# Performance work log

Hardware: AMD Instinct MI355X
Metric: run time of the kernel (lower is better)

## Reference

```python
import jax, jax.numpy as jnp
import numpy as np

TOP_K = 10
RANKING_WEIGHT = 0.3
UP_WEIGHT = 1.0
DOWN_WEIGHT = 0.5
NEG = 1e9  # finite stand-in for -inf so softmax/grads stay NaN-free


def setup_inputs() -> dict:
    key = jax.random.key(0)
    k1, k2, k3, k4 = jax.random.split(key, 4)
    B, N = 1024, 5000
    up_logits = jax.random.normal(k1, (B, N), jnp.float32)
    down_logits = jax.random.normal(k2, (B, N), jnp.float32)
    y_true = jax.random.normal(k3, (B, N), jnp.float32) * 0.05  # daily returns
    masks = jax.random.randint(k4, (B, N), 0, 2).astype(jnp.int32)
    return {"up_logits": up_logits, "down_logits": down_logits,
            "y_true": y_true, "masks": masks}


def _bce_with_logits(x, z):
    # softplus(x) - x*z  ==  -[z*log(sig(x)) + (1-z)*log(1-sig(x))]
    return jax.nn.softplus(x) - x * z


def reference(up_logits, down_logits, y_true, masks):
    maskb = masks > 0                                   # [B, N]
    maskf = maskb.astype(up_logits.dtype)
    num_valid = maskf.sum(-1)                           # [B]
    nv_safe = jnp.maximum(num_valid, 1.0)
    k = jnp.minimum(TOP_K, num_valid.astype(jnp.int32))  # [B] min(top_k, num)

    # Descending rank of y_true among valid entries (invalid pushed to bottom).
    y_desc = jnp.where(maskb, y_true, -NEG)
    rank_desc = jnp.argsort(jnp.argsort(-y_desc, axis=-1), axis=-1)  # [B, N]
    up_labels = (rank_desc < k[:, None]).astype(up_logits.dtype)

    # Ascending rank (biggest losers) for down path.
    y_asc = jnp.where(maskb, y_true, NEG)
    rank_asc = jnp.argsort(jnp.argsort(y_asc, axis=-1), axis=-1)
    down_labels = (rank_asc < k[:, None]).astype(down_logits.dtype)

    # Mean BCE over valid entries per row.
    up_loss = jnp.sum(_bce_with_logits(up_logits, up_labels) * maskf, -1) / nv_safe
    down_loss = jnp.sum(_bce_with_logits(down_logits, down_labels) * maskf, -1) / nv_safe

    # Listwise KL: softmax over valid entries; kl_div(log p, q, 'batchmean')
    # with 1D input of size num divides the sum by num.
    logp = jax.nn.log_softmax(jnp.where(maskb, up_logits, -NEG), axis=-1)
    logq = jax.nn.log_softmax(jnp.where(maskb, y_true, -NEG), axis=-1)
    q = jnp.exp(logq)
    kl = jnp.sum(jnp.where(maskb, q * (logq - logp), 0.0), -1) / nv_safe

    batch_loss = UP_WEIGHT * up_loss + DOWN_WEIGHT * down_loss + RANKING_WEIGHT * kl
    batch_loss = jnp.where(num_valid > 0, batch_loss, 0.0)  # skip empty rows
    return jnp.sum(batch_loss) / up_logits.shape[0]
```

## Files before the change

### kernel.cpp

```cpp
#include <hip/hip_runtime.h>
#include <math.h>

#define NCOLS 5000
#define NF4   1250
#define BLOCK 640
#define NWAVES (BLOCK / 64)
#define NITER 2
#define TOPKK 10
#define CAP 384

__device__ __forceinline__ unsigned mono_f32(float f) {
  unsigned u = __float_as_uint(f);
  return (u & 0x80000000u) ? ~u : (u | 0x80000000u);
}

__device__ __forceinline__ float wave_sum_f(float v) {
#pragma unroll
  for (int o = 1; o < 64; o <<= 1) v += __shfl_xor(v, o);
  return v;
}
__device__ __forceinline__ int wave_sum_i(int v) {
#pragma unroll
  for (int o = 1; o < 64; o <<= 1) v += __shfl_xor(v, o);
  return v;
}
__device__ __forceinline__ unsigned wave_max_u(unsigned v) {
#pragma unroll
  for (int o = 1; o < 64; o <<= 1) {
    unsigned w = __shfl_xor(v, o);
    v = w > v ? w : v;
  }
  return v;
}

extern "C" __global__ __launch_bounds__(BLOCK, 8)
void row_loss_kernel(const float* __restrict__ up, const float* __restrict__ down,
                     const float* __restrict__ yt, const int* __restrict__ masks,
                     float* __restrict__ out, float inv_nrows) {
  __shared__ float red_f[6][NWAVES];
  __shared__ int red_i[NWAVES];
  __shared__ unsigned t1w_t[NWAVES];
  __shared__ unsigned t1w_b[NWAVES];
  __shared__ unsigned keys_t[CAP];
  __shared__ int      col_t[CAP];
  __shared__ unsigned keys_b[CAP];
  __shared__ int      col_b[CAP];
  __shared__ int ct, cb;
  __shared__ float s_res[2];

  const int tid = threadIdx.x;
  const int lane = tid & 63;
  const int wv = tid >> 6;
  const int row = blockIdx.x;
  const long long b4 = (long long)row * NF4;
  const long long base = (long long)row * NCOLS;

  const float4* up4 = (const float4*)up + b4;
  const float4* dn4 = (const float4*)down + b4;
  const float4* yt4 = (const float4*)yt + b4;
  const int4*   mk4 = (const int4*)masks + b4;

  if (tid == 0) { ct = 0; cb = 0; }

  unsigned km[NITER][4];
  int nv_l = 0;
  float sq = 0.f, sp = 0.f, seyy = 0.f, seyu = 0.f;
  float pu = 1.f, pd = 1.f;
  unsigned a0 = 0u, a1 = 0u, bb0 = 0u, bb1 = 0u;
#pragma unroll
  for (int j = 0; j < NITER; ++j) {
    const int f = j * BLOCK + tid;
    const int fc = f < NF4 ? f : NF4 - 1;
    const float4 y4 = yt4[fc];
    const float4 u4 = up4[fc];
    const float4 d4 = dn4[fc];
    const int4   m4 = mk4[fc];
    const bool inb = f < NF4;
    const float* yp = (const float*)&y4;
    const float* upp = (const float*)&u4;
    const float* dp = (const float*)&d4;
    const int* mp = (const int*)&m4;
#pragma unroll
    for (int c = 0; c < 4; ++c) {
      const bool valid = inb && (mp[c] > 0);
      const float y = yp[c], u = upp[c], d = dp[c];
      const unsigned kd = valid ? mono_f32(y) : 0u;
      const unsigned kb = valid ? ~kd : 0u;
      km[j][c] = kd;
      if (kd > a1) { if (kd > a0) { a1 = a0; a0 = kd; } else a1 = kd; }
      if (kb > bb1) { if (kb > bb0) { bb1 = bb0; bb0 = kb; } else bb1 = kb; }
      const float ey = __expf(y);
      const float eu = __expf(u);
      const float ed = __expf(d);
      nv_l += valid ? 1 : 0;
      sq   += valid ? ey : 0.f;
      seyy += valid ? ey * y : 0.f;
      seyu += valid ? ey * u : 0.f;
      sp   += valid ? eu : 0.f;
      pu   *= valid ? (1.f + eu) : 1.f;
      pd   *= valid ? (1.f + ed) : 1.f;
    }
  }
  float aspu = __logf(pu);
  float aspd = __logf(pd);

  nv_l = wave_sum_i(nv_l);
  sq = wave_sum_f(sq);
  sp = wave_sum_f(sp);
  seyy = wave_sum_f(seyy);
  seyu = wave_sum_f(seyu);
  aspu = wave_sum_f(aspu);
  aspd = wave_sum_f(aspd);
  if (lane == 0) {
    red_i[wv] = nv_l;
    red_f[0][wv] = sq;  red_f[1][wv] = sp;
    red_f[2][wv] = seyy; red_f[3][wv] = seyu;
    red_f[4][wv] = aspu; red_f[5][wv] = aspd;
  }

  {
    unsigned v0 = a0, v1 = a1, t1 = 0u;
#pragma unroll 1
    for (int r = 0; r < TOPKK; ++r) {
      unsigned m = wave_max_u(v0 > v1 ? v0 : v1);
      if (v0 == m) v0 = 0u;
      else if (v1 == m) v1 = 0u;
      t1 = m;
    }
    if (lane == 0) t1w_t[wv] = t1;
  }
  {
    unsigned v0 = bb0, v1 = bb1, t1 = 0u;
#pragma unroll 1
    for (int r = 0; r < TOPKK; ++r) {
      unsigned m = wave_max_u(v0 > v1 ? v0 : v1);
      if (v0 == m) v0 = 0u;
      else if (v1 == m) v1 = 0u;
      t1 = m;
    }
    if (lane == 0) t1w_b[wv] = t1;
  }
  __syncthreads();

  int nv = 0;
#pragma unroll
  for (int w = 0; w < NWAVES; ++w) nv += red_i[w];
  const int k = nv < TOPKK ? nv : TOPKK;

  unsigned t1 = 0u, t1b = 0u;
#pragma unroll
  for (int w = 0; w < NWAVES; ++w) {
    t1 = t1w_t[w] > t1 ? t1w_t[w] : t1;
    t1b = t1w_b[w] > t1b ? t1w_b[w] : t1b;
  }

#pragma unroll
  for (int j = 0; j < NITER; ++j) {
#pragma unroll
    for (int c = 0; c < 4; ++c) {
      const unsigned kd = km[j][c];
      if (kd != 0u) {
        const int col = ((j * BLOCK + tid) << 2) + c;
        if (kd >= t1) {
          int i = atomicAdd(&ct, 1);
          if (i < CAP) { keys_t[i] = kd; col_t[i] = col; }
        }
        const unsigned kb = ~kd;
        if (kb >= t1b) {
          int i = atomicAdd(&cb, 1);
          if (i < CAP) { keys_b[i] = kb; col_b[i] = col; }
        }
      }
    }
  }
  __syncthreads();

  if (wv == 0) {
    const int n = ct < CAP ? ct : CAP;
    unsigned kk[6];
#pragma unroll
    for (int i = 0; i < 6; ++i) {
      const int idx = i * 64 + lane;
      kk[i] = (idx < n) ? keys_t[idx] : 0u;
    }
    unsigned w0 = kk[0], w1 = kk[1], w2 = kk[2], w3 = kk[3], w4 = kk[4], w5 = kk[5];
    unsigned thr = 0xFFFFFFFFu;
#pragma unroll 1
    for (int r = 0; r < k; ++r) {
      unsigned l0 = w0 > w1 ? w0 : w1;
      unsigned l1 = w2 > w3 ? w2 : w3;
      unsigned l2 = w4 > w5 ? w4 : w5;
      l0 = l0 > l1 ? l0 : l1;
      unsigned m = wave_max_u(l0 > l2 ? l0 : l2);
      if (w0 == m) w0 = 0u;
      else if (w1 == m) w1 = 0u;
      else if (w2 == m) w2 = 0u;
      else if (w3 == m) w3 = 0u;
      else if (w4 == m) w4 = 0u;
      else if (w5 == m) w5 = 0u;
      thr = m;
    }
    float su = 0.f;
#pragma unroll
    for (int i = 0; i < 6; ++i) {
      const int idx = i * 64 + lane;
      if (kk[i] >= thr && kk[i] != 0u) su += up[base + col_t[idx]];
    }
    su = wave_sum_f(su);
    if (lane == 0) s_res[0] = su;
  } else if (wv == 1) {
    const int n = cb < CAP ? cb : CAP;
    unsigned kk[6];
#pragma unroll
    for (int i = 0; i < 6; ++i) {
      const int idx = i * 64 + lane;
      kk[i] = (idx < n) ? keys_b[idx] : 0u;
    }
    unsigned w0 = kk[0], w1 = kk[1], w2 = kk[2], w3 = kk[3], w4 = kk[4], w5 = kk[5];
    unsigned thr = 0xFFFFFFFFu;
#pragma unroll 1
    for (int r = 0; r < k; ++r) {
      unsigned l0 = w0 > w1 ? w0 : w1;
      unsigned l1 = w2 > w3 ? w2 : w3;
      unsigned l2 = w4 > w5 ? w4 : w5;
      l0 = l0 > l1 ? l0 : l1;
      unsigned m = wave_max_u(l0 > l2 ? l0 : l2);
      if (w0 == m) w0 = 0u;
      else if (w1 == m) w1 = 0u;
      else if (w2 == m) w2 = 0u;
      else if (w3 == m) w3 = 0u;
      else if (w4 == m) w4 = 0u;
      else if (w5 == m) w5 = 0u;
      thr = m;
    }
    float sd = 0.f;
#pragma unroll
    for (int i = 0; i < 6; ++i) {
      const int idx = i * 64 + lane;
      if (kk[i] >= thr && kk[i] != 0u) sd += down[base + col_b[idx]];
    }
    sd = wave_sum_f(sd);
    if (lane == 0) s_res[1] = sd;
  }
  __syncthreads();

  if (tid == 0 && nv > 0) {
    float SQ = 0.f, SP = 0.f, SYY = 0.f, SYU = 0.f, ASU = 0.f, ASD = 0.f;
#pragma unroll
    for (int w = 0; w < NWAVES; ++w) {
      SQ += red_f[0][w]; SP += red_f[1][w];
      SYY += red_f[2][w]; SYU += red_f[3][w];
      ASU += red_f[4][w]; ASD += red_f[5][w];
    }
    const float SU = s_res[0];
    const float SD = s_res[1];
    const float kl = (SYY - SYU) / SQ - __logf(SQ) + __logf(SP);
    const float up_loss = ASU - SU;
    const float dn_loss = ASD - SD;
    const float loss = (up_loss + 0.5f * dn_loss + 0.3f * kl) / (float)nv;
    atomicAdd(out, loss * inv_nrows);
  }
}

extern "C" void kernel_launch(void* const* d_in, const int* in_sizes, int n_in,
                              void* d_out, int out_size, void* d_ws, size_t ws_size,
                              hipStream_t stream) {
  const float* up_logits   = (const float*)d_in[0];
  const float* down_logits = (const float*)d_in[1];
  const float* y_true      = (const float*)d_in[2];
  const int*   masks       = (const int*)d_in[3];

  const int nrows = in_sizes[0] / NCOLS;

  hipMemsetAsync(d_out, 0, sizeof(float) * (size_t)out_size, stream);
  row_loss_kernel<<<nrows, BLOCK, 0, stream>>>(up_logits, down_logits, y_true,
                                               masks, (float*)d_out,
                                               1.0f / (float)nrows);
}
```

Measured before the change: 135.3 us.

## Use 256-thread blocks with 5 iterations and per-thread max for top-k threshold

Shrinks the block from 640 to 256 threads so each thread handles 20 elements instead of 8. Each thread now keeps only its single max key rather than its top two, which makes the per-wave 10th-max threshold a looser but still valid lower bound. Invalid entries are clamped to -1000 before exponentiation so the accumulations can drop their select operations. The softplus product is split into two partial products so it does not overflow over 20 factors. With a looser threshold, more candidates may land in shared memory and the CAP of 384 is more likely to overflow; the smaller block also changes occupancy and load parallelism per row.

```diff
diff --git a/kernel.cpp b/kernel.cpp
--- a/kernel.cpp
+++ b/kernel.cpp
@@ -3,9 +3,9 @@
 
 #define NCOLS 5000
 #define NF4   1250
-#define BLOCK 640
+#define BLOCK 256
 #define NWAVES (BLOCK / 64)
-#define NITER 2
+#define NITER 5
 #define TOPKK 10
 #define CAP 384
 
@@ -33,7 +33,7 @@
   return v;
 }
 
-extern "C" __global__ __launch_bounds__(BLOCK, 8)
+extern "C" __global__ __launch_bounds__(BLOCK, 4)
 void row_loss_kernel(const float* __restrict__ up, const float* __restrict__ down,
                      const float* __restrict__ yt, const int* __restrict__ masks,
                      float* __restrict__ out, float inv_nrows) {
@@ -65,8 +65,8 @@
   unsigned km[NITER][4];
   int nv_l = 0;
   float sq = 0.f, sp = 0.f, seyy = 0.f, seyu = 0.f;
-  float pu = 1.f, pd = 1.f;
-  unsigned a0 = 0u, a1 = 0u, bb0 = 0u, bb1 = 0u;
+  float pu0 = 1.f, pu1 = 1.f, pd0 = 1.f, pd1 = 1.f;
+  unsigned tmax = 0u, tbmax = 0u;
 #pragma unroll
   for (int j = 0; j < NITER; ++j) {
     const int f = j * BLOCK + tid;
@@ -83,26 +83,28 @@
 #pragma unroll
     for (int c = 0; c < 4; ++c) {
       const bool valid = inb && (mp[c] > 0);
-      const float y = yp[c], u = upp[c], d = dp[c];
+      const float y = valid ? yp[c] : -1000.f;
+      const float u = valid ? upp[c] : -1000.f;
+      const float d = valid ? dp[c] : -1000.f;
       const unsigned kd = valid ? mono_f32(y) : 0u;
       const unsigned kb = valid ? ~kd : 0u;
       km[j][c] = kd;
-      if (kd > a1) { if (kd > a0) { a1 = a0; a0 = kd; } else a1 = kd; }
-      if (kb > bb1) { if (kb > bb0) { bb1 = bb0; bb0 = kb; } else bb1 = kb; }
+      tmax = kd > tmax ? kd : tmax;
+      tbmax = kb > tbmax ? kb : tbmax;
+      nv_l += valid ? 1 : 0;
       const float ey = __expf(y);
       const float eu = __expf(u);
       const float ed = __expf(d);
-      nv_l += valid ? 1 : 0;
-      sq   += valid ? ey : 0.f;
-      seyy += valid ? ey * y : 0.f;
-      seyu += valid ? ey * u : 0.f;
-      sp   += valid ? eu : 0.f;
-      pu   *= valid ? (1.f + eu) : 1.f;
-      pd   *= valid ? (1.f + ed) : 1.f;
-    }
-  }
-  float aspu = __logf(pu);
-  float aspd = __logf(pd);
+      sq += ey;
+      seyy += ey * y;
+      seyu += ey * u;
+      sp += eu;
+      if (j < 3) { pu0 *= 1.f + eu; pd0 *= 1.f + ed; }
+      else       { pu1 *= 1.f + eu; pd1 *= 1.f + ed; }
+    }
+  }
+  float aspu = __logf(pu0) + __logf(pu1);
+  float aspd = __logf(pd0) + __logf(pd1);
 
   nv_l = wave_sum_i(nv_l);
   sq = wave_sum_f(sq);
@@ -119,23 +121,21 @@
   }
 
   {
-    unsigned v0 = a0, v1 = a1, t1 = 0u;
+    unsigned v = tmax, t1 = 0u;
 #pragma unroll 1
     for (int r = 0; r < TOPKK; ++r) {
-      unsigned m = wave_max_u(v0 > v1 ? v0 : v1);
-      if (v0 == m) v0 = 0u;
-      else if (v1 == m) v1 = 0u;
+      unsigned m = wave_max_u(v);
+      if (v == m) v = 0u;
       t1 = m;
     }
     if (lane == 0) t1w_t[wv] = t1;
   }
   {
-    unsigned v0 = bb0, v1 = bb1, t1 = 0u;
+    unsigned v = tbmax, t1 = 0u;
 #pragma unroll 1
     for (int r = 0; r < TOPKK; ++r) {
-      unsigned m = wave_max_u(v0 > v1 ? v0 : v1);
-      if (v0 == m) v0 = 0u;
-      else if (v1 == m) v1 = 0u;
+      unsigned m = wave_max_u(v);
+      if (v == m) v = 0u;
       t1 = m;
     }
     if (lane == 0) t1w_b[wv] = t1;
```

Result: faster. 125.0 us (-7.6%).
